# Kernel optimization log

Hardware: AMD Instinct MI355X
Metric: run time of the kernel (lower is better)

## Reference

```python
import jax, jax.numpy as jnp
import numpy as np

N_NODES = 50000
N_EDGES = 800000
N_GRAPHS = 256


def setup_inputs() -> dict:
    key = jax.random.key(0)
    ks = jax.random.split(key, 20)
    s = 0.05
    return {
        "x": jax.random.normal(ks[0], (N_NODES, 128), jnp.float32),
        "edge_index": jax.random.randint(ks[1], (2, N_EDGES), 0, N_NODES, jnp.int64),
        "batch_index": jnp.sort(jax.random.randint(ks[2], (N_NODES,), 0, N_GRAPHS, jnp.int64)),
        "mol_features": jax.random.normal(ks[3], (N_GRAPHS, 256), jnp.float32),
        "gcn_W": jax.random.normal(ks[4], (3, 128, 128), jnp.float32) * s,
        "gcn_b": jax.random.normal(ks[5], (3, 128), jnp.float32) * s,
        "gcn_out_W": jax.random.normal(ks[6], (128, 128), jnp.float32) * s,
        "gcn_out_b": jax.random.normal(ks[7], (128,), jnp.float32) * s,
        "mlp_W": jax.random.normal(ks[8], (2, 256, 256), jnp.float32) * s,
        "mlp_b": jax.random.normal(ks[9], (2, 256), jnp.float32) * s,
        "mlp_out_W": jax.random.normal(ks[10], (64, 256), jnp.float32) * s,
        "mlp_out_b": jax.random.normal(ks[11], (64,), jnp.float32) * s,
        "pred_W1": jax.random.normal(ks[12], (256, 192), jnp.float32) * s,
        "pred_b1": jax.random.normal(ks[13], (256,), jnp.float32) * s,
        "pred_W2": jax.random.normal(ks[14], (256, 256), jnp.float32) * s,
        "pred_b2": jax.random.normal(ks[15], (256,), jnp.float32) * s,
        "out_W": jax.random.normal(ks[16], (1, 256), jnp.float32) * s,
        "out_b": jax.random.normal(ks[17], (1,), jnp.float32) * s,
    }


def reference(x, edge_index, batch_index, mol_features,
              gcn_W, gcn_b, gcn_out_W, gcn_out_b,
              mlp_W, mlp_b, mlp_out_W, mlp_out_b,
              pred_W1, pred_b1, pred_W2, pred_b2, out_W, out_b):
    N = x.shape[0]
    E = edge_index.shape[1]
    G = mol_features.shape[0]
    row, col = edge_index[0], edge_index[1]

    # GCN normalization with self-loops (PyG gcn_norm, symmetric):
    # deg[i] = in-degree(i) + 1 (self loop); norm_e = d^-1/2[row] * d^-1/2[col]
    deg = jax.ops.segment_sum(jnp.ones((E,), x.dtype), col, num_segments=N) + 1.0
    dinv = jax.lax.rsqrt(deg)
    enorm = (dinv[row] * dinv[col])[:, None]     # [E,1]
    self_c = (dinv * dinv)[:, None]              # [N,1] self-loop coefficient

    h1 = x
    for i in range(gcn_W.shape[0]):
        h = h1 @ gcn_W[i].T                      # per-node transform [N,128]
        agg = jax.ops.segment_sum(h[row] * enorm, col, num_segments=N)
        h1 = jax.nn.relu(agg + self_c * h + gcn_b[i])
    h1 = h1 @ gcn_out_W.T + gcn_out_b            # final GCN-branch Linear (no relu)

    # global_mean_pool over batch_index -> [G,128]
    sums = jax.ops.segment_sum(h1, batch_index, num_segments=G)
    counts = jax.ops.segment_sum(jnp.ones((N,), x.dtype), batch_index, num_segments=G)
    h1 = sums / jnp.maximum(counts, 1.0)[:, None]

    # MLP branch: relu after every linear (including last)
    h2 = mol_features
    for i in range(mlp_W.shape[0]):
        h2 = jax.nn.relu(h2 @ mlp_W[i].T + mlp_b[i])
    h2 = jax.nn.relu(h2 @ mlp_out_W.T + mlp_out_b)

    h = jnp.concatenate([h1, h2], axis=1)        # [G,192]
    h = jax.nn.relu(h @ pred_W1.T + pred_b1)
    h = jax.nn.relu(h @ pred_W2.T + pred_b2)
    return h @ out_W.T + out_b                   # [G,1]
```

## Files before the change

### kernel.cpp

```cpp
#include <hip/hip_runtime.h>


typedef __attribute__((ext_vector_type(8))) short short8;
typedef __attribute__((ext_vector_type(4))) float f32x4;

#define BKT 64
#define SL 16
#define CAP 192
#define WCAP 2560
#define NBINBLK 2048
#define HROWS 65536

#define HW_MLP0 0
#define HW_MLP1 65536
#define HW_MLO  131072
#define HW_GCNO 147456
#define HW_PW1  163840
#define HW_PW2  212992
#define HW_TOT  278528

__device__ __forceinline__ unsigned short f2bf(float f) {
    union { float f; unsigned u; } c; c.f = f;
    unsigned u = c.u;
    unsigned r = u + 0x7FFFu + ((u >> 16) & 1u);
    return (unsigned short)(r >> 16);
}
__device__ __forceinline__ float bflo(unsigned w) {
    union { unsigned u; float f; } c; c.u = w << 16; return c.f;
}
__device__ __forceinline__ float bfhi(unsigned w) {
    union { unsigned u; float f; } c; c.u = w & 0xFFFF0000u; return c.f;
}

__global__ void k_init(int* cur, float* pool, float* cnt,
                       const float* __restrict__ gcnW, uint4* __restrict__ Wb,
                       const float* __restrict__ mlpW, const float* __restrict__ mloW,
                       const float* __restrict__ gcnoW, const float* __restrict__ pW1,
                       const float* __restrict__ pW2, unsigned short* __restrict__ Wh,
                       int M, int G) {
    int i = blockIdx.x * 256 + threadIdx.x;
    if (i < M * 16) cur[i] = 0;
    if (i < G * 128) pool[i] = 0.f;
    if (i < G) cnt[i] = 0.f;
    if (i < 3 * 2048) {
        int l = i >> 11, rem = i & 2047;
        int o = rem >> 4, c = rem & 15;
        const float4* s = (const float4*)(gcnW + (size_t)l * 16384 + o * 128 + c * 8);
        float4 a = s[0], b = s[1];
        uint4 v;
        v.x = ((unsigned)f2bf(a.y) << 16) | f2bf(a.x);
        v.y = ((unsigned)f2bf(a.w) << 16) | f2bf(a.z);
        v.z = ((unsigned)f2bf(b.y) << 16) | f2bf(b.x);
        v.w = ((unsigned)f2bf(b.w) << 16) | f2bf(b.z);
        Wb[(l << 11) | (o << 4) | (c ^ (o & 15))] = v;
    }
    int j = i - 8192;
    if (j >= 0 && j < (HW_TOT / 8)) {
        int e = j * 8;
        const float* src;
        if (e < HW_MLO)        src = mlpW  + e;
        else if (e < HW_GCNO)  src = mloW  + (e - HW_MLO);
        else if (e < HW_PW1)   src = gcnoW + (e - HW_GCNO);
        else if (e < HW_PW2)   src = pW1   + (e - HW_PW1);
        else                   src = pW2   + (e - HW_PW2);
        float4 a = *(const float4*)src;
        float4 b = *((const float4*)src + 1);
        uint4 v;
        v.x = ((unsigned)f2bf(a.y) << 16) | f2bf(a.x);
        v.y = ((unsigned)f2bf(a.w) << 16) | f2bf(a.z);
        v.z = ((unsigned)f2bf(b.y) << 16) | f2bf(b.x);
        v.w = ((unsigned)f2bf(b.w) << 16) | f2bf(b.z);
        *(uint4*)(Wh + e) = v;
    }
}

__global__ __launch_bounds__(256) void k_bin(const int* __restrict__ row,
                                             const int* __restrict__ col,
                                             int* __restrict__ cur,
                                             unsigned* __restrict__ gbin,
                                             int E, int C) {
    const int x = blockIdx.x & (SL - 1);
    int e0 = blockIdx.x * C, e1 = min(E, e0 + C);
    for (int e = e0 + threadIdx.x; e < e1; e += 256) {
        int c = col[e];
        int cell = (c >> 6) * SL + x;
        int cnt = atomicAdd(&cur[cell << 4], 1);
        gbin[cell * CAP + cnt] = (unsigned)row[e] | ((unsigned)(c & 63) << 16);
    }
}

__global__ __launch_bounds__(256) void k_csr(const unsigned* __restrict__ gbin,
                                             const int* __restrict__ cur,
                                             int* __restrict__ rs,
                                             unsigned short* __restrict__ rd,
                                             float* __restrict__ dinv,
                                             unsigned short* __restrict__ csrf,
                                             const float* __restrict__ x,
                                             unsigned short* __restrict__ xb,
                                             int N) {
    const int b = blockIdx.x, t = threadIdx.x;
    __shared__ int hcnt[64], lcur[64], fills[SL];
    __shared__ float sdinv[64];
    if (t < 64) hcnt[t] = 0;
    if (t < SL) fills[t] = cur[(b * SL + t) << 4];
    __syncthreads();
    #pragma unroll 4
    for (int xx = 0; xx < SL; ++xx) {
        int cbase = (b * SL + xx) * CAP, fill = fills[xx];
        for (int i = t; i < fill; i += 256)
            atomicAdd(&hcnt[(gbin[cbase + i] >> 16) & 63], 1);
    }
    __syncthreads();
    if (t < 64) {
        int v = hcnt[t], xs = v;
        #pragma unroll
        for (int off = 1; off < 64; off <<= 1) {
            int u = __shfl_up(xs, off, 64);
            if (t >= off) xs += u;
        }
        int excl = xs - v;
        lcur[t] = excl;
        float d = rsqrtf((float)v + 1.0f);
        sdinv[t] = d;
        int node = b * 64 + t;
        rs[node] = b * WCAP + excl;
        rd[node] = (unsigned short)v;
        dinv[node] = d;
    }
    __syncthreads();
    #pragma unroll 4
    for (int xx = 0; xx < SL; ++xx) {
        int cbase = (b * SL + xx) * CAP, fill = fills[xx];
        for (int i = t; i < fill; i += 256) {
            unsigned v = gbin[cbase + i];
            int p = atomicAdd(&lcur[(v >> 16) & 63], 1);
            csrf[b * WCAP + p] = (unsigned short)(v & 0xFFFFu);
        }
    }
    const int node0 = b * 64;
    #pragma unroll
    for (int it = 0; it < 4; ++it) {
        int i = t + it * 256;
        int nd = node0 + (i >> 4);
        if (nd < N) {
            int ch = i & 15;
            float d = sdinv[i >> 4];
            const float4* s = (const float4*)(x + (size_t)nd * 128 + ch * 8);
            float4 a = s[0], bb = s[1];
            uint4 o;
            o.x = ((unsigned)f2bf(d * a.y) << 16) | f2bf(d * a.x);
            o.y = ((unsigned)f2bf(d * a.w) << 16) | f2bf(d * a.z);
            o.z = ((unsigned)f2bf(d * bb.y) << 16) | f2bf(d * bb.x);
            o.w = ((unsigned)f2bf(d * bb.w) << 16) | f2bf(d * bb.z);
            *(uint4*)(xb + (size_t)nd * 128 + ch * 8) = o;
        }
    }
}

__global__ __launch_bounds__(1024, 8) void k_fused(
    const unsigned short* __restrict__ h,
    const uint4* __restrict__ Wb,
    const float* __restrict__ bias,
    const float* __restrict__ dscale,
    const float* __restrict__ dinv,
    const int* __restrict__ rs,
    const unsigned short* __restrict__ rd,
    const unsigned short* __restrict__ csrf,
    unsigned short* __restrict__ C, int N) {
    __shared__ uint4 Wsh[2048];
    __shared__ unsigned short Ash[64][136];

    const int t = threadIdx.x;
    Wsh[t] = Wb[t];
    Wsh[t + 1024] = Wb[t + 1024];

    const int lane = t & 63;
    const int wv = t >> 6;
    const int fg = lane & 15;
    const int slot = lane >> 4;

    for (int s = 0; s < 4; ++s) {
        const int lrow = wv * 4 + s;
        const int n = blockIdx.x * 64 + lrow;
        if (n < N) {
            const int st = rs[n], e = st + rd[n];
            float acc[8] = {0.f, 0.f, 0.f, 0.f, 0.f, 0.f, 0.f, 0.f};
            for (int base = st; base < e; base += 16) {
                int src_l = csrf[base + fg];
                #pragma unroll
                for (int i = 0; i < 4; ++i) {
                    int j = i * 4 + slot;
                    bool ok = (base + j) < e;
                    int src = __shfl(src_l, j, 16);
                    src = ok ? src : 0;
                    uint4 v = *(const uint4*)(h + (size_t)src * 128 + fg * 8);
                    v.x = ok ? v.x : 0u; v.y = ok ? v.y : 0u;
                    v.z = ok ? v.z : 0u; v.w = ok ? v.w : 0u;
                    acc[0] += bflo(v.x); acc[1] += bfhi(v.x);
                    acc[2] += bflo(v.y); acc[3] += bfhi(v.y);
                    acc[4] += bflo(v.z); acc[5] += bfhi(v.z);
                    acc[6] += bflo(v.w); acc[7] += bfhi(v.w);
                }
            }
            #pragma unroll
            for (int r = 0; r < 8; ++r) {
                acc[r] += __shfl_xor(acc[r], 16, 64);
                acc[r] += __shfl_xor(acc[r], 32, 64);
            }
            if (slot == 0) {
                float dn = dinv[n];
                uint4 hv = *(const uint4*)(h + (size_t)n * 128 + fg * 8);
                float sv[8] = {bflo(hv.x), bfhi(hv.x), bflo(hv.y), bfhi(hv.y),
                               bflo(hv.z), bfhi(hv.z), bflo(hv.w), bfhi(hv.w)};
                unsigned short ob[8];
                #pragma unroll
                for (int r = 0; r < 8; ++r) ob[r] = f2bf(dn * (acc[r] + sv[r]));
                uint4 o;
                o.x = ((unsigned)ob[1] << 16) | ob[0];
                o.y = ((unsigned)ob[3] << 16) | ob[2];
                o.z = ((unsigned)ob[5] << 16) | ob[4];
                o.w = ((unsigned)ob[7] << 16) | ob[6];
                *(uint4*)(&Ash[lrow][fg * 8]) = o;
            }
        } else if (slot == 0) {
            uint4 z = {0u, 0u, 0u, 0u};
            *(uint4*)(&Ash[lrow][fg * 8]) = z;
        }
    }
    __syncthreads();

    const int rt = wv & 3, cp = wv >> 2;
    const int l15 = fg, quad = slot;
    f32x4 acc2[2];
    acc2[0] = (f32x4){0.f, 0.f, 0.f, 0.f};
    acc2[1] = (f32x4){0.f, 0.f, 0.f, 0.f};
    #pragma unroll
    for (int kiter = 0; kiter < 4; ++kiter) {
        short8 af = *(const short8*)(&Ash[rt * 16 + l15][kiter * 32 + quad * 8]);
        const int cswz = (kiter * 4 + quad) ^ l15;
        #pragma unroll
        for (int cc = 0; cc < 2; ++cc) {
            int ct = cp * 2 + cc;
            short8 bf = *(const short8*)(&Wsh[((ct * 16 + l15) << 4) | cswz]);
            acc2[cc] = __builtin_amdgcn_mfma_f32_16x16x32_bf16(af, bf, acc2[cc], 0, 0, 0);
        }
    }

    const int rbase = blockIdx.x * 64 + rt * 16 + quad * 4;
    float ds[4];
    #pragma unroll
    for (int r = 0; r < 4; ++r) {
        int rr = rbase + r;
        ds[r] = (dscale && rr < N) ? dscale[rr] : 1.f;
    }
    #pragma unroll
    for (int cc = 0; cc < 2; ++cc) {
        int colc = (cp * 2 + cc) * 16 + l15;
        float bcol = bias[colc];
        #pragma unroll
        for (int r = 0; r < 4; ++r) {
            int rr = rbase + r;
            if (rr < N) {
                float v = fmaxf(acc2[cc][r] + bcol, 0.f) * ds[r];
                C[(size_t)rr * 128 + colc] = f2bf(v);
            }
        }
    }
}

__global__ __launch_bounds__(256) void k_pool(const unsigned short* __restrict__ h,
                                              const int* __restrict__ batch,
                                              float* __restrict__ pool,
                                              float* __restrict__ cnt, int N) {
    int t = threadIdx.x;
    int fg = t & 15, sg = t >> 4;
    int n0 = blockIdx.x * 512 + sg * 32;
    if (n0 >= N) return;
    int n1 = min(n0 + 32, N);
    int gprev = batch[n0];
    float racc[8] = {0.f, 0.f, 0.f, 0.f, 0.f, 0.f, 0.f, 0.f};
    float rcnt = 0.f;
    for (int n = n0; n < n1; ++n) {
        int g = batch[n];
        if (g != gprev) {
            float* dst = pool + (size_t)gprev * 128 + fg * 8;
            #pragma unroll
            for (int r = 0; r < 8; ++r) atomicAdd(dst + r, racc[r]);
            if (fg == 0) atomicAdd(&cnt[gprev], rcnt);
            #pragma unroll
            for (int r = 0; r < 8; ++r) racc[r] = 0.f;
            rcnt = 0.f; gprev = g;
        }
        uint4 v = *(const uint4*)(h + (size_t)n * 128 + fg * 8);
        racc[0] += bflo(v.x); racc[1] += bfhi(v.x);
        racc[2] += bflo(v.y); racc[3] += bfhi(v.y);
        racc[4] += bflo(v.z); racc[5] += bfhi(v.z);
        racc[6] += bflo(v.w); racc[7] += bfhi(v.w);
        rcnt += 1.f;
    }
    float* dst = pool + (size_t)gprev * 128 + fg * 8;
    #pragma unroll
    for (int r = 0; r < 8; ++r) atomicAdd(dst + r, racc[r]);
    if (fg == 0) atomicAdd(&cnt[gprev], rcnt);
}

__global__ __launch_bounds__(256) void k_head(
    const unsigned short* __restrict__ Wh,
    const float* __restrict__ pool, const float* __restrict__ cnt,
    const float* __restrict__ mol,
    const float* __restrict__ mlpb, const float* __restrict__ mlob,
    const float* __restrict__ gcnob,
    const float* __restrict__ pb1, const float* __restrict__ pb2,
    const float* __restrict__ oW, const float* __restrict__ ob,
    float* __restrict__ out, int G) {
    const int g0 = blockIdx.x * 16;
    const int t = threadIdx.x;
    const int lane = t & 63, wv = t >> 6;
    const int l15 = lane & 15, quad = lane >> 4;
    __shared__ unsigned short A[16][264], B[16][264], Cc[16][200], Mn[16][136];
    __shared__ float red[4][16];

    for (int i = t; i < 16 * 256; i += 256) {
        int g = i >> 8, k = i & 255;
        A[g][k] = f2bf(mol[(size_t)(g0 + g) * 256 + k]);
    }
    for (int i = t; i < 16 * 128; i += 256) {
        int g = i >> 7, k = i & 127;
        float c = cnt[g0 + g];
        Mn[g][k] = f2bf(pool[(size_t)(g0 + g) * 128 + k] / fmaxf(c, 1.f));
    }
    __syncthreads();

    auto do_tile = [&](const unsigned short* actb, int astr, int K,
                       const unsigned short* W, int orow,
                       const float* __restrict__ bias, int bidx,
                       unsigned short* dstb, int dstr, int ocol, bool dorelu) {
        f32x4 c = {0.f, 0.f, 0.f, 0.f};
        for (int kt = 0; kt < (K >> 5); ++kt) {
            short8 af = *(const short8*)(actb + (size_t)l15 * astr + kt * 32 + quad * 8);
            short8 bf = *(const short8*)(W + (size_t)orow * K + kt * 32 + quad * 8);
            c = __builtin_amdgcn_mfma_f32_16x16x32_bf16(af, bf, c, 0, 0, 0);
        }
        float bb = bias[bidx];
        #pragma unroll
        for (int r = 0; r < 4; ++r) {
            int g = quad * 4 + r;
            float v = c[r] + bb;
            if (dorelu) v = fmaxf(v, 0.f);
            dstb[(size_t)g * dstr + ocol] = f2bf(v);
        }
    };

    #pragma unroll
    for (int nt = 0; nt < 4; ++nt) {
        int o = (wv * 4 + nt) * 16 + l15;
        do_tile(&A[0][0], 264, 256, Wh + HW_MLP0, o, mlpb, o, &B[0][0], 264, o, true);
    }
    __syncthreads();
    #pragma unroll
    for (int nt = 0; nt < 4; ++nt) {
        int o = (wv * 4 + nt) * 16 + l15;
        do_tile(&B[0][0], 264, 256, Wh + HW_MLP1, o, mlpb + 256, o, &A[0][0], 264, o, true);
    }
    __syncthreads();
    #pragma unroll
    for (int j = 0; j < 3; ++j) {
        int tile = wv * 3 + j;
        if (tile < 8) {
            int o = tile * 16 + l15;
            do_tile(&Mn[0][0], 136, 128, Wh + HW_GCNO, o, gcnob, o, &Cc[0][0], 200, o, false);
        } else {
            int om = (tile - 8) * 16 + l15;
            do_tile(&A[0][0], 264, 256, Wh + HW_MLO, om, mlob, om, &Cc[0][0], 200, 128 + om, true);
        }
    }
    __syncthreads();
    #pragma unroll
    for (int nt = 0; nt < 4; ++nt) {
        int o = (wv * 4 + nt) * 16 + l15;
        do_tile(&Cc[0][0], 200, 192, Wh + HW_PW1, o, pb1, o, &B[0][0], 264, o, true);
    }
    __syncthreads();
    {
        float pacc[4] = {0.f, 0.f, 0.f, 0.f};
        #pragma unroll
        for (int nt = 0; nt < 4; ++nt) {
            int o = (wv * 4 + nt) * 16 + l15;
            f32x4 c = {0.f, 0.f, 0.f, 0.f};
            #pragma unroll
            for (int kt = 0; kt < 8; ++kt) {
                short8 af = *(const short8*)(&B[0][0] + (size_t)l15 * 264 + kt * 32 + quad * 8);
                short8 bf = *(const short8*)(Wh + HW_PW2 + (size_t)o * 256 + kt * 32 + quad * 8);
                c = __builtin_amdgcn_mfma_f32_16x16x32_bf16(af, bf, c, 0, 0, 0);
            }
            float bb = pb2[o], wo = oW[o];
            #pragma unroll
            for (int r = 0; r < 4; ++r)
                pacc[r] += fmaxf(c[r] + bb, 0.f) * wo;
        }
        #pragma unroll
        for (int off = 1; off < 16; off <<= 1)
            #pragma unroll
            for (int r = 0; r < 4; ++r)
                pacc[r] += __shfl_xor(pacc[r], off, 64);
        if (l15 == 0) {
            #pragma unroll
            for (int r = 0; r < 4; ++r)
                red[wv][quad * 4 + r] = pacc[r];
        }
    }
    __syncthreads();
    if (t < 16) {
        float s = red[0][t] + red[1][t] + red[2][t] + red[3][t] + ob[0];
        if (g0 + t < G) out[g0 + t] = s;
    }
}

extern "C" void kernel_launch(void* const* d_in, const int* in_sizes, int n_in,
                              void* d_out, int out_size, void* d_ws, size_t ws_size,
                              hipStream_t stream) {
    const float* x     = (const float*)d_in[0];
    const int*   ei    = (const int*)d_in[1];
    const int*   batch = (const int*)d_in[2];
    const float* mol   = (const float*)d_in[3];
    const float* gcnW  = (const float*)d_in[4];
    const float* gcnb  = (const float*)d_in[5];
    const float* gcnoW = (const float*)d_in[6];
    const float* gcnob = (const float*)d_in[7];
    const float* mlpW  = (const float*)d_in[8];
    const float* mlpb  = (const float*)d_in[9];
    const float* mloW  = (const float*)d_in[10];
    const float* mlob  = (const float*)d_in[11];
    const float* pW1   = (const float*)d_in[12];
    const float* pb1   = (const float*)d_in[13];
    const float* pW2   = (const float*)d_in[14];
    const float* pb2   = (const float*)d_in[15];
    const float* oW    = (const float*)d_in[16];
    const float* ob    = (const float*)d_in[17];

    const int N = in_sizes[0] / 128;
    const int E = in_sizes[1] / 2;
    const int G = in_sizes[3] / 256;
    const int* row = ei;
    const int* col = ei + E;

    const int NBK = (N + BKT - 1) / BKT;
    const int M = NBK * SL;
    const int C = (E + NBINBLK - 1) / NBINBLK;

    char* p = (char*)d_ws;
    auto alloc = [&](size_t bytes) {
        char* q = p;
        p += (bytes + 255) & ~(size_t)255;
        return (void*)q;
    };
    int*    rs    = (int*)alloc((size_t)NBK * 64 * 4);
    unsigned short* rd = (unsigned short*)alloc((size_t)NBK * 64 * 2);
    float*  dinv  = (float*)alloc((size_t)NBK * 64 * 4);
    int*    cur   = (int*)alloc((size_t)M * 16 * 4);
    unsigned* gbin = (unsigned*)alloc((size_t)M * CAP * 4);
    unsigned short* csrf = (unsigned short*)alloc(((size_t)NBK * WCAP + 32) * 2);
    unsigned short* xb   = (unsigned short*)alloc((size_t)HROWS * 128 * 2);
    unsigned short* bufA = (unsigned short*)alloc((size_t)HROWS * 128 * 2);
    unsigned short* bufB = (unsigned short*)alloc((size_t)HROWS * 128 * 2);
    uint4*  Wb    = (uint4*)alloc((size_t)3 * 2048 * 16);
    unsigned short* Wh = (unsigned short*)alloc((size_t)HW_TOT * 2);
    float*  pool  = (float*)alloc((size_t)G * 128 * 4);
    float*  cnt   = (float*)alloc((size_t)G * 4);

    const int initblocks = (M * 16 + 255) / 256;

    k_init<<<initblocks, 256, 0, stream>>>(cur, pool, cnt, gcnW, Wb,
                                           mlpW, mloW, gcnoW, pW1, pW2, Wh, M, G);
    k_bin<<<NBINBLK, 256, 0, stream>>>(row, col, cur, gbin, E, C);
    k_csr<<<NBK, 256, 0, stream>>>(gbin, cur, rs, rd, dinv, csrf, x, xb, N);

    const int fblocks = (N + 63) / 64;
    unsigned short* dst[3] = {bufA, bufB, bufA};
    const unsigned short* src = xb;
    for (int l = 0; l < 3; ++l) {
        k_fused<<<fblocks, 1024, 0, stream>>>(src, Wb + (size_t)l * 2048,
                                              gcnb + (size_t)l * 128,
                                              (l < 2) ? dinv : (const float*)nullptr,
                                              dinv, rs, rd, csrf, dst[l], N);
        src = dst[l];
    }
    k_pool<<<(N + 511) / 512, 256, 0, stream>>>(bufA, batch, pool, cnt, N);
    k_head<<<(G + 15) / 16, 256, 0, stream>>>(
        Wh, pool, cnt, mol, mlpb, mlob, gcnob, pb1, pb2, oW, ob,
        (float*)d_out, G);
}
```

Baseline: 338.2 us.

## Pad CSR rows to 8 with zero sentinel, one node per 16 lanes, fuse pooling

Each node's neighbor list is padded to a multiple of 8, and the padding slots point at an extra all-zero row N, so the gather loop needs no bounds masks and can load 8 neighbor ids at once. Each 16-lane group now handles one node for the whole gather, which removes the cross-slot shuffle reduction. The mean-pool sum moves into the last GCN layer's epilogue as per-graph atomics, and the per-graph node counts move into the CSR kernel, so the separate pool kernel and the final layer's write-out disappear. In exchange, high-degree nodes may cause load imbalance within a block, the launch bound now allows fewer blocks per CU, and more atomics hit the pool buffer.

```diff
diff --git a/kernel.cpp b/kernel.cpp
--- a/kernel.cpp
+++ b/kernel.cpp
@@ -2,6 +2,7 @@
 
 
 typedef __attribute__((ext_vector_type(8))) short short8;
+typedef __attribute__((ext_vector_type(8))) unsigned short ushort8;
 typedef __attribute__((ext_vector_type(4))) float f32x4;
 
 #define BKT 64
@@ -37,11 +38,16 @@
                        const float* __restrict__ mlpW, const float* __restrict__ mloW,
                        const float* __restrict__ gcnoW, const float* __restrict__ pW1,
                        const float* __restrict__ pW2, unsigned short* __restrict__ Wh,
-                       int M, int G) {
+                       unsigned short* xb, unsigned short* bufA, unsigned short* bufB,
+                       int M, int G, int N) {
     int i = blockIdx.x * 256 + threadIdx.x;
     if (i < M * 16) cur[i] = 0;
     if (i < G * 128) pool[i] = 0.f;
     if (i < G) cnt[i] = 0.f;
+    if (i < 192) {
+        unsigned short* b = (i < 64) ? xb : (i < 128) ? bufA : bufB;
+        *(unsigned*)(b + (size_t)N * 128 + (i & 63) * 2) = 0u;
+    }
     if (i < 3 * 2048) {
         int l = i >> 11, rem = i & 2047;
         int o = rem >> 4, c = rem & 15;
@@ -97,7 +103,8 @@
                                              unsigned short* __restrict__ csrf,
                                              const float* __restrict__ x,
                                              unsigned short* __restrict__ xb,
-                                             int N) {
+                                             const int* __restrict__ batch,
+                                             float* __restrict__ cnt, int N) {
     const int b = blockIdx.x, t = threadIdx.x;
     __shared__ int hcnt[64], lcur[64], fills[SL];
     __shared__ float sdinv[64];
@@ -112,13 +119,15 @@
     }
     __syncthreads();
     if (t < 64) {
-        int v = hcnt[t], xs = v;
+        int v = hcnt[t];
+        int vp = (v + 7) & ~7;
+        int xs = vp;
         #pragma unroll
         for (int off = 1; off < 64; off <<= 1) {
             int u = __shfl_up(xs, off, 64);
             if (t >= off) xs += u;
         }
-        int excl = xs - v;
+        int excl = xs - vp;
         lcur[t] = excl;
         float d = rsqrtf((float)v + 1.0f);
         sdinv[t] = d;
@@ -126,6 +135,7 @@
         rs[node] = b * WCAP + excl;
         rd[node] = (unsigned short)v;
         dinv[node] = d;
+        if (node < N) atomicAdd(&cnt[batch[node]], 1.f);
     }
     __syncthreads();
     #pragma unroll 4
@@ -136,6 +146,13 @@
             int p = atomicAdd(&lcur[(v >> 16) & 63], 1);
             csrf[b * WCAP + p] = (unsigned short)(v & 0xFFFFu);
         }
+    }
+    __syncthreads();
+    if (t < 64) {
+        int v = hcnt[t], vp = (v + 7) & ~7;
+        int base = lcur[t];
+        for (int p = v; p < vp; ++p)
+            csrf[b * WCAP + base + (p - v)] = (unsigned short)N;
     }
     const int node0 = b * 64;
     #pragma unroll
@@ -157,7 +174,7 @@
     }
 }
 
-__global__ __launch_bounds__(1024, 8) void k_fused(
+__global__ __launch_bounds__(1024, 4) void k_fused(
     const unsigned short* __restrict__ h,
     const uint4* __restrict__ Wb,
     const float* __restrict__ bias,
@@ -166,7 +183,9 @@
     const int* __restrict__ rs,
     const unsigned short* __restrict__ rd,
     const unsigned short* __restrict__ csrf,
-    unsigned short* __restrict__ C, int N) {
+    unsigned short* __restrict__ C,
+    const int* __restrict__ batch,
+    float* __restrict__ pool, int N) {
     __shared__ uint4 Wsh[2048];
     __shared__ unsigned short Ash[64][136];
 
@@ -174,63 +193,52 @@
     Wsh[t] = Wb[t];
     Wsh[t + 1024] = Wb[t + 1024];
 
+    const int sub = t >> 4;
+    const int fg = t & 15;
+    const int blk0 = blockIdx.x * 64;
+    const int node = blk0 + sub;
+
+    float acc[8] = {0.f, 0.f, 0.f, 0.f, 0.f, 0.f, 0.f, 0.f};
+    if (node < N) {
+        uint4 hv = *(const uint4*)(h + (size_t)node * 128 + fg * 8);
+        acc[0] = bflo(hv.x); acc[1] = bfhi(hv.x);
+        acc[2] = bflo(hv.y); acc[3] = bfhi(hv.y);
+        acc[4] = bflo(hv.z); acc[5] = bfhi(hv.z);
+        acc[6] = bflo(hv.w); acc[7] = bfhi(hv.w);
+    }
+    {
+        const int st = rs[node];
+        const int ep = st + ((rd[node] + 7) & ~7);
+        for (int i = st; i < ep; i += 8) {
+            ushort8 ids = *(const ushort8*)(csrf + i);
+            #pragma unroll
+            for (int k = 0; k < 8; ++k) {
+                uint4 v = *(const uint4*)(h + (size_t)ids[k] * 128 + fg * 8);
+                acc[0] += bflo(v.x); acc[1] += bfhi(v.x);
+                acc[2] += bflo(v.y); acc[3] += bfhi(v.y);
+                acc[4] += bflo(v.z); acc[5] += bfhi(v.z);
+                acc[6] += bflo(v.w); acc[7] += bfhi(v.w);
+            }
+        }
+    }
+    {
+        const float dn = (node < N) ? dinv[node] : 0.f;
+        unsigned short ob[8];
+        #pragma unroll
+        for (int j = 0; j < 8; ++j) ob[j] = f2bf(acc[j] * dn);
+        uint4 o;
+        o.x = ((unsigned)ob[1] << 16) | ob[0];
+        o.y = ((unsigned)ob[3] << 16) | ob[2];
+        o.z = ((unsigned)ob[5] << 16) | ob[4];
+        o.w = ((unsigned)ob[7] << 16) | ob[6];
+        *(uint4*)(&Ash[sub][fg * 8]) = o;
+    }
+    __syncthreads();
+
     const int lane = t & 63;
     const int wv = t >> 6;
-    const int fg = lane & 15;
-    const int slot = lane >> 4;
-
-    for (int s = 0; s < 4; ++s) {
-        const int lrow = wv * 4 + s;
-        const int n = blockIdx.x * 64 + lrow;
-        if (n < N) {
-            const int st = rs[n], e = st + rd[n];
-            float acc[8] = {0.f, 0.f, 0.f, 0.f, 0.f, 0.f, 0.f, 0.f};
-            for (int base = st; base < e; base += 16) {
-                int src_l = csrf[base + fg];
-                #pragma unroll
-                for (int i = 0; i < 4; ++i) {
-                    int j = i * 4 + slot;
-                    bool ok = (base + j) < e;
-                    int src = __shfl(src_l, j, 16);
-                    src = ok ? src : 0;
-                    uint4 v = *(const uint4*)(h + (size_t)src * 128 + fg * 8);
-                    v.x = ok ? v.x : 0u; v.y = ok ? v.y : 0u;
-                    v.z = ok ? v.z : 0u; v.w = ok ? v.w : 0u;
-                    acc[0] += bflo(v.x); acc[1] += bfhi(v.x);
-                    acc[2] += bflo(v.y); acc[3] += bfhi(v.y);
-                    acc[4] += bflo(v.z); acc[5] += bfhi(v.z);
-                    acc[6] += bflo(v.w); acc[7] += bfhi(v.w);
-                }
-            }
-            #pragma unroll
-            for (int r = 0; r < 8; ++r) {
-                acc[r] += __shfl_xor(acc[r], 16, 64);
-                acc[r] += __shfl_xor(acc[r], 32, 64);
-            }
-            if (slot == 0) {
-                float dn = dinv[n];
-                uint4 hv = *(const uint4*)(h + (size_t)n * 128 + fg * 8);
-                float sv[8] = {bflo(hv.x), bfhi(hv.x), bflo(hv.y), bfhi(hv.y),
-                               bflo(hv.z), bfhi(hv.z), bflo(hv.w), bfhi(hv.w)};
-                unsigned short ob[8];
-                #pragma unroll
-                for (int r = 0; r < 8; ++r) ob[r] = f2bf(dn * (acc[r] + sv[r]));
-                uint4 o;
-                o.x = ((unsigned)ob[1] << 16) | ob[0];
-                o.y = ((unsigned)ob[3] << 16) | ob[2];
-                o.z = ((unsigned)ob[5] << 16) | ob[4];
-                o.w = ((unsigned)ob[7] << 16) | ob[6];
-                *(uint4*)(&Ash[lrow][fg * 8]) = o;
-            }
-        } else if (slot == 0) {
-            uint4 z = {0u, 0u, 0u, 0u};
-            *(uint4*)(&Ash[lrow][fg * 8]) = z;
-        }
-    }
-    __syncthreads();
-
+    const int l15 = lane & 15, quad = lane >> 4;
     const int rt = wv & 3, cp = wv >> 2;
-    const int l15 = fg, quad = slot;
     f32x4 acc2[2];
     acc2[0] = (f32x4){0.f, 0.f, 0.f, 0.f};
     acc2[1] = (f32x4){0.f, 0.f, 0.f, 0.f};
@@ -246,62 +254,51 @@
         }
     }
 
-    const int rbase = blockIdx.x * 64 + rt * 16 + quad * 4;
-    float ds[4];
-    #pragma unroll
-    for (int r = 0; r < 4; ++r) {
-        int rr = rbase + r;
-        ds[r] = (dscale && rr < N) ? dscale[rr] : 1.f;
-    }
-    #pragma unroll
-    for (int cc = 0; cc < 2; ++cc) {
-        int colc = (cp * 2 + cc) * 16 + l15;
-        float bcol = bias[colc];
+    const int rbase = blk0 + rt * 16 + quad * 4;
+    if (pool) {
+        int gr[4];
+        #pragma unroll
+        for (int r = 0; r < 4; ++r)
+            gr[r] = (rbase + r < N) ? batch[rbase + r] : -1;
+        #pragma unroll
+        for (int cc = 0; cc < 2; ++cc) {
+            int colc = (cp * 2 + cc) * 16 + l15;
+            float bcol = bias[colc];
+            float s = 0.f; int gprev = -2;
+            #pragma unroll
+            for (int r = 0; r < 4; ++r) {
+                if (gr[r] >= 0) {
+                    float v = fmaxf(acc2[cc][r] + bcol, 0.f);
+                    if (gr[r] == gprev) s += v;
+                    else {
+                        if (gprev >= 0) atomicAdd(&pool[(size_t)gprev * 128 + colc], s);
+                        gprev = gr[r]; s = v;
+                    }
+                }
+            }
+            if (gprev >= 0) atomicAdd(&pool[(size_t)gprev * 128 + colc], s);
+        }
+    } else {
+        float ds[4];
         #pragma unroll
         for (int r = 0; r < 4; ++r) {
             int rr = rbase + r;
-            if (rr < N) {
-                float v = fmaxf(acc2[cc][r] + bcol, 0.f) * ds[r];
-                C[(size_t)rr * 128 + colc] = f2bf(v);
+            ds[r] = (dscale && rr < N) ? dscale[rr] : 1.f;
+        }
+        #pragma unroll
+        for (int cc = 0; cc < 2; ++cc) {
+            int colc = (cp * 2 + cc) * 16 + l15;
+            float bcol = bias[colc];
+            #pragma unroll
+            for (int r = 0; r < 4; ++r) {
+                int rr = rbase + r;
+                if (rr < N) {
+                    float v = fmaxf(acc2[cc][r] + bcol, 0.f) * ds[r];
+                    C[(size_t)rr * 128 + colc] = f2bf(v);
+                }
             }
         }
     }
-}
-
-__global__ __launch_bounds__(256) void k_pool(const unsigned short* __restrict__ h,
-                                              const int* __restrict__ batch,
-                                              float* __restrict__ pool,
-                                              float* __restrict__ cnt, int N) {
-    int t = threadIdx.x;
-    int fg = t & 15, sg = t >> 4;
-    int n0 = blockIdx.x * 512 + sg * 32;
-    if (n0 >= N) return;
-    int n1 = min(n0 + 32, N);
-    int gprev = batch[n0];
-    float racc[8] = {0.f, 0.f, 0.f, 0.f, 0.f, 0.f, 0.f, 0.f};
-    float rcnt = 0.f;
-    for (int n = n0; n < n1; ++n) {
-        int g = batch[n];
-        if (g != gprev) {
-            float* dst = pool + (size_t)gprev * 128 + fg * 8;
-            #pragma unroll
-            for (int r = 0; r < 8; ++r) atomicAdd(dst + r, racc[r]);
-            if (fg == 0) atomicAdd(&cnt[gprev], rcnt);
-            #pragma unroll
-            for (int r = 0; r < 8; ++r) racc[r] = 0.f;
-            rcnt = 0.f; gprev = g;
-        }
-        uint4 v = *(const uint4*)(h + (size_t)n * 128 + fg * 8);
-        racc[0] += bflo(v.x); racc[1] += bfhi(v.x);
-        racc[2] += bflo(v.y); racc[3] += bfhi(v.y);
-        racc[4] += bflo(v.z); racc[5] += bfhi(v.z);
-        racc[6] += bflo(v.w); racc[7] += bfhi(v.w);
-        rcnt += 1.f;
-    }
-    float* dst = pool + (size_t)gprev * 128 + fg * 8;
-    #pragma unroll
-    for (int r = 0; r < 8; ++r) atomicAdd(dst + r, racc[r]);
-    if (fg == 0) atomicAdd(&cnt[gprev], rcnt);
 }
 
 __global__ __launch_bounds__(256) void k_head(
@@ -471,21 +468,23 @@
     const int initblocks = (M * 16 + 255) / 256;
 
     k_init<<<initblocks, 256, 0, stream>>>(cur, pool, cnt, gcnW, Wb,
-                                           mlpW, mloW, gcnoW, pW1, pW2, Wh, M, G);
+                                           mlpW, mloW, gcnoW, pW1, pW2, Wh,
+                                           xb, bufA, bufB, M, G, N);
     k_bin<<<NBINBLK, 256, 0, stream>>>(row, col, cur, gbin, E, C);
-    k_csr<<<NBK, 256, 0, stream>>>(gbin, cur, rs, rd, dinv, csrf, x, xb, N);
+    k_csr<<<NBK, 256, 0, stream>>>(gbin, cur, rs, rd, dinv, csrf, x, xb,
+                                   batch, cnt, N);
 
     const int fblocks = (N + 63) / 64;
-    unsigned short* dst[3] = {bufA, bufB, bufA};
-    const unsigned short* src = xb;
-    for (int l = 0; l < 3; ++l) {
-        k_fused<<<fblocks, 1024, 0, stream>>>(src, Wb + (size_t)l * 2048,
-                                              gcnb + (size_t)l * 128,
-                                              (l < 2) ? dinv : (const float*)nullptr,
-                                              dinv, rs, rd, csrf, dst[l], N);
-        src = dst[l];
-    }
-    k_pool<<<(N + 511) / 512, 256, 0, stream>>>(bufA, batch, pool, cnt, N);
+    k_fused<<<fblocks, 1024, 0, stream>>>(xb, Wb, gcnb, dinv, dinv,
+                                          rs, rd, csrf, bufA,
+                                          batch, (float*)nullptr, N);
+    k_fused<<<fblocks, 1024, 0, stream>>>(bufA, Wb + 2048, gcnb + 128, dinv, dinv,
+                                          rs, rd, csrf, bufB,
+                                          batch, (float*)nullptr, N);
+    k_fused<<<fblocks, 1024, 0, stream>>>(bufB, Wb + 4096, gcnb + 256,
+                                          (const float*)nullptr, dinv,
+                                          rs, rd, csrf, bufA,
+                                          batch, pool, N);
     k_head<<<(G + 15) / 16, 256, 0, stream>>>(
         Wh, pool, cnt, mol, mlpb, mlob, gcnob, pb1, pb2, oW, ob,
         (float*)d_out, G);
```

Result: slower. 406.5 us (+20.2%).
